# Optimization experiments

Measured on AMD Instinct MI355X. Metric: run time of the kernel, lower is better.

## Reference

```python
import jax, jax.numpy as jnp
import numpy as np

N = 50000; E = 800000; T = 800000; G = 64
H = 128; IEMB = 128; BAS = 8; NS = 4; NR = 6; OEH = 128; OUT = 1; NB = 4; CUT = 5.0


def envelope(x):
    # exponent=5 -> p=6: 1/x + a*x^5 + b*x^6 + c*x^7 with a=-28, b=48, c=-21
    return 1.0 / x - 28.0 * x**5 + 48.0 * x**6 - 21.0 * x**7


def setup_inputs() -> dict:
    key = jax.random.key(0)
    ks = iter(jax.random.split(key, 80))
    def w(shape, s=0.1):
        return jax.random.normal(next(ks), shape, dtype=jnp.float32) * s
    inp = {}
    inp['z'] = jax.random.randint(next(ks), (N,), 0, 100, dtype=jnp.int32)
    inp['dist'] = jax.random.uniform(next(ks), (E,), jnp.float32, 0.05, 1.0)
    inp['dist_trip'] = jax.random.uniform(next(ks), (T,), jnp.float32, 0.05, 1.0)
    inp['angle'] = jax.random.uniform(next(ks), (T,), jnp.float32, -1.0, 1.0)
    inp['edge_index'] = jax.random.randint(next(ks), (2, E), 0, N, dtype=jnp.int32)
    inp['triplets'] = jax.random.randint(next(ks), (T, 3), 0, N, dtype=jnp.int32)
    inp['batch'] = jnp.sort(jax.random.randint(next(ks), (N,), 0, G, dtype=jnp.int32))
    inp['atom_table'] = w((100, H), 1.0)
    inp['rbf_freq'] = jnp.arange(1, NR + 1, dtype=jnp.float32) * jnp.float32(np.pi)
    inp['sbf_freq'] = jnp.arange(1, NR + 1, dtype=jnp.float32) * jnp.float32(np.pi)
    inp['emb_w1'] = w((NR, IEMB)); inp['emb_b1'] = w((IEMB,), 0.01)
    inp['emb_w2'] = w((IEMB, H)); inp['emb_b2'] = w((H,), 0.01)
    inp['iw_rbf1'] = w((NB, NR, BAS)); inp['iw_rbf2'] = w((NB, BAS, H))
    inp['iw_sbf1'] = w((NB, NS * NR, BAS)); inp['iw_sbf2'] = w((NB, BAS, IEMB))
    inp['iw_t1'] = w((NB, H, IEMB)); inp['iw_t2'] = w((NB, IEMB, H)); inp['ib_t2'] = w((NB, H), 0.01)
    inp['iw_up'] = w((NB, H, H)); inp['ib_up'] = w((NB, H), 0.01)
    inp['iw_down'] = w((NB, H, H)); inp['ib_down'] = w((NB, H), 0.01)
    inp['ow_rbf'] = w((NB + 1, NR, H))
    inp['ow0'] = w((NB + 1, H, OEH)); inp['ob0'] = w((NB + 1, OEH), 0.01)
    inp['ow1'] = w((NB + 1, OEH, OEH)); inp['ob1'] = w((NB + 1, OEH), 0.01)
    inp['ow2'] = w((NB + 1, OEH, OUT)); inp['ob2'] = w((NB + 1, OUT), 0.01)
    return inp


def _forward(atom_table, rbf_freq, sbf_freq, emb_w1, emb_b1, emb_w2, emb_b2,
             iw_rbf1, iw_rbf2, iw_sbf1, iw_sbf2, iw_t1, iw_t2, ib_t2,
             iw_up, ib_up, iw_down, ib_down, ow_rbf, ow0, ob0, ow1, ob1, ow2, ob2,
             dist, dist_trip, angle, z, edge_index, triplets, batch):
    row, col = edge_index[0], edge_index[1]
    j_idx = triplets[:, 1]
    # radial basis for edges: [E, NR]
    d = dist[:, None] / CUT
    rbf_e = envelope(d) * jnp.sin(rbf_freq * d)
    # spherical basis for triplets: [T, NS*NR]
    dt = dist_trip[:, None] / CUT
    rbf_t = envelope(dt) * jnp.sin(sbf_freq * dt)
    a = angle[:, None]
    sph = jnp.concatenate([jnp.ones_like(a), a, 0.5 * (3 * a**2 - 1), 0.5 * (5 * a**3 - 3 * a)], axis=-1)
    sbf_t = (rbf_t[:, None, :] * sph[:, :, None]).reshape(a.shape[0], -1)

    x = atom_table[z]  # [N, H]
    # EmbeddingBlock: edge msg from rbf only, scattered to col
    e = jax.nn.silu(rbf_e @ emb_w1 + emb_b1) @ emb_w2 + emb_b2
    x = x + jax.ops.segment_sum(e, col, num_segments=N)

    def out_block(k, x):
        rbf_emb = rbf_e @ ow_rbf[k]            # [E, H]
        h = jax.ops.segment_sum(x[row] * rbf_emb, col, num_segments=N)
        h = jax.nn.silu(h @ ow0[k] + ob0[k])
        h = jax.nn.silu(h @ ow1[k] + ob1[k])
        return h @ ow2[k] + ob2[k]             # [N, OUT]

    P = out_block(0, x)
    for b in range(NB):
        x_up = x @ iw_up[b] + ib_up[b]
        x_down = x @ iw_down[b] + ib_down[b]
        rbf_emb = jax.nn.silu(rbf_e @ iw_rbf1[b]) @ iw_rbf2[b]      # [E, H]
        x_edge = x_up[row] * rbf_emb                                  # [E, H]
        sbf_emb = jax.nn.silu(sbf_t @ iw_sbf1[b]) @ iw_sbf2[b]      # [T, H]
        t = jax.nn.silu(x_down @ iw_t1[b]) @ iw_t2[b] + ib_t2[b]     # [N, H]
        # original: for each triplet i, x_edge += t[j]*sbf_emb[i] (broadcast over all edges)
        extra = jnp.sum(t[j_idx] * sbf_emb, axis=0)                   # [H]
        x_edge = x_edge + extra
        x = x + jax.ops.segment_sum(x_edge, col, num_segments=N)
        P = P + out_block(b + 1, x)

    counts = jax.ops.segment_sum(jnp.ones((x.shape[0],), jnp.float32), batch, num_segments=G)
    pooled = jax.ops.segment_sum(P, batch, num_segments=G) / jnp.maximum(counts, 1.0)[:, None]
    return pooled  # [G, OUT]


def reference(z, dist, dist_trip, angle, edge_index, triplets, batch, atom_table, rbf_freq, sbf_freq,
              emb_w1, emb_b1, emb_w2, emb_b2, iw_rbf1, iw_rbf2, iw_sbf1, iw_sbf2, iw_t1, iw_t2, ib_t2,
              iw_up, ib_up, iw_down, ib_down, ow_rbf, ow0, ob0, ow1, ob1, ow2, ob2):
    return _forward(atom_table, rbf_freq, sbf_freq, emb_w1, emb_b1, emb_w2, emb_b2,
                    iw_rbf1, iw_rbf2, iw_sbf1, iw_sbf2, iw_t1, iw_t2, ib_t2,
                    iw_up, ib_up, iw_down, ib_down, ow_rbf, ow0, ob0, ow1, ob1, ow2, ob2,
                    dist, dist_trip, angle, z, edge_index, triplets, batch)
```

## Files before the change

### kernel.cpp

```cpp
#include <hip/hip_runtime.h>
#include <hip/hip_fp16.h>

#define N_ 50000
#define E_ 800000
#define T_ 800000
#define G_ 64
#define H_ 128

#define NBK 782
#define NSB (NBK * 8)
#define CAPS 512
#define CHUNK 4096
#define EB ((E_ + CHUNK - 1) / CHUNK)
#define TB ((T_ + CHUNK - 1) / CHUNK)
#define XSLOT 16

#define GEMMG2 ((N_ + 31) / 32)
#define NG2 ((N_ + 1) / 2)
#define NIX ((N_ * 16 + 127) / 128)
#define SVG ((N_ + 3) / 4)
#define EG ((E_ + 255) / 256)
#define TG ((T_ + 255) / 256)

typedef __attribute__((ext_vector_type(8))) short bf16x8;
typedef __attribute__((ext_vector_type(4))) float f32x4;
typedef _Float16 f16x2 __attribute__((ext_vector_type(2)));

__device__ __forceinline__ float siluf(float v) {
    return __fdividef(v, 1.0f + __expf(-v));
}

__device__ __forceinline__ unsigned short f2bf(float f) {
    unsigned int u = __float_as_uint(f);
    u += 0x7fffu + ((u >> 16) & 1u);
    return (unsigned short)(u >> 16);
}
__device__ __forceinline__ unsigned int f2bf2(float a, float b) {
    return (unsigned int)f2bf(a) | ((unsigned int)f2bf(b) << 16);
}
__device__ __forceinline__ float bf2f(unsigned short h) {
    return __uint_as_float(((unsigned int)h) << 16);
}
__device__ __forceinline__ float2 bf2x2(unsigned int p) {
    return make_float2(__uint_as_float(p << 16), __uint_as_float(p & 0xffff0000u));
}
__device__ __forceinline__ float fdot2f(f16x2 a, f16x2 b, float c) {
    return __builtin_amdgcn_fdot2(a, b, c, false);
}

__global__ __launch_bounds__(256) void k_bucket(const int* __restrict__ ecol,
                                                const int* __restrict__ trip,
                                                int* bcntE, unsigned int* __restrict__ ebkt,
                                                int* bcntT, unsigned int* __restrict__ tbkt) {
    __shared__ int hist[NBK];
    __shared__ int bbase[NBK];
    int blk = blockIdx.x;
    bool isE = blk < EB;
    int ebase = (isE ? blk : blk - EB) * CHUNK;
    const int nElem = isE ? E_ : T_;
    int r = blk & 7;
    int* bcnt = isE ? bcntE : bcntT;
    unsigned int* bkt = isE ? ebkt : tbkt;
    int tid = threadIdx.x;

    for (int i = tid; i < NBK; i += 256) hist[i] = 0;
    __syncthreads();

    int cols[16];
    #pragma unroll
    for (int u = 0; u < 16; ++u) {
        int idx = ebase + u * 256 + tid;
        int c = -1;
        if (idx < nElem) c = isE ? ecol[idx] : trip[3 * idx + 1];
        cols[u] = c;
        if (c >= 0) atomicAdd(&hist[c >> 6], 1);
    }
    __syncthreads();

    for (int b = tid; b < NBK; b += 256) {
        int c = hist[b];
        bbase[b] = c ? atomicAdd(&bcnt[b * 8 + r], c) : 0;
        hist[b] = 0;
    }
    __syncthreads();

    #pragma unroll
    for (int u = 0; u < 16; ++u) {
        int c = cols[u];
        if (c >= 0) {
            int bk = c >> 6;
            int off = atomicAdd(&hist[bk], 1);
            int pos = bbase[bk] + off;
            if (pos < CAPS) {
                int idx = ebase + u * 256 + tid;
                bkt[(size_t)(bk * 8 + r) * CAPS + pos] =
                    ((unsigned int)idx << 6) | (unsigned int)(c & 63);
            }
        }
    }
}

// ... 143 lines not shown
        if (t >= T_) return;
        float2 da = tpay[t];
        float d = da.x * 0.2f;
        float a = da.y;
        float d2 = d * d, d4 = d2 * d2, d5 = d4 * d;
        float env = __fdividef(1.0f, d) - 28.0f * d5 + 48.0f * d5 * d - 21.0f * d5 * d2;
        float rb[6];
        #pragma unroll
        for (int r = 0; r < 6; ++r) rb[r] = env * __sinf(sfreq[r] * d);
        float sph[4];
        sph[0] = 1.0f; sph[1] = a; sph[2] = 1.5f * a * a - 0.5f; sph[3] = 2.5f * a * a * a - 1.5f * a;
        __half out[24];
        #pragma unroll
        for (int s = 0; s < 4; ++s)
            #pragma unroll
            for (int r = 0; r < 6; ++r) out[s * 6 + r] = __float2half(sph[s] * rb[r]);
        uint4* dst = (uint4*)(basis + (size_t)t * 24);
        dst[0] = ((uint4*)out)[0];
        dst[1] = ((uint4*)out)[1];
        dst[2] = ((uint4*)out)[2];
    }
}

__global__ __launch_bounds__(128) void k_embSix(const float* __restrict__ atab, const int* __restrict__ z,
                                                unsigned short* __restrict__ xh,
                                                const int* __restrict__ rowptr, const float* __restrict__ rbfS,
                                                const float* __restrict__ w1, const float* __restrict__ b1,
                                                unsigned short* __restrict__ SSh) {
    int tid = threadIdx.x;
    if (blockIdx.x < NIX) {
        int t = blockIdx.x * 128 + tid;
        if (t >= N_ * 16) return;
        int node = t >> 4, q = t & 15;
        const float4* a4 = (const float4*)atab;
        float4 v0 = a4[(size_t)z[node] * 32 + q * 2];
        float4 v1 = a4[(size_t)z[node] * 32 + q * 2 + 1];
        uint4 pk;
        pk.x = f2bf2(v0.x, v0.y);
        pk.y = f2bf2(v0.z, v0.w);
        pk.z = f2bf2(v1.x, v1.y);
        pk.w = f2bf2(v1.z, v1.w);
        ((uint4*)xh)[t] = pk;
    } else {
        int node = (blockIdx.x - NIX) * 2 + (tid >> 6);
        int lane = tid & 63;
        if (node >= N_) return;
        int c = lane * 2;
        float wc0[6], wc1[6];
        #pragma unroll
        for (int r = 0; r < 6; ++r) { wc0[r] = w1[r * 128 + c]; wc1[r] = w1[r * 128 + c + 1]; }
        float bb0 = b1[c], bb1 = b1[c + 1];
        float a0 = 0.f, a1 = 0.f;
        int p0 = rowptr[node], p1 = rowptr[node + 1];
        int p = p0;
        for (; p + 4 <= p1; p += 4) {
            float2 rb[4][3];
            #pragma unroll
            for (int u = 0; u < 4; ++u) {
                const float2* r2 = (const float2*)&rbfS[(size_t)(p + u) * 6];
                rb[u][0] = r2[0]; rb[u][1] = r2[1]; rb[u][2] = r2[2];
            }
            #pragma unroll
            for (int u = 0; u < 4; ++u) {
                float u0 = bb0 + rb[u][0].x * wc0[0] + rb[u][0].y * wc0[1] + rb[u][1].x * wc0[2] +
                           rb[u][1].y * wc0[3] + rb[u][2].x * wc0[4] + rb[u][2].y * wc0[5];
                float u1 = bb1 + rb[u][0].x * wc1[0] + rb[u][0].y * wc1[1] + rb[u][1].x * wc1[2] +
                           rb[u][1].y * wc1[3] + rb[u][2].x * wc1[4] + rb[u][2].y * wc1[5];
                a0 += siluf(u0);
                a1 += siluf(u1);
            }
        }
        for (; p < p1; ++p) {
            const float2* r2 = (const float2*)&rbfS[(size_t)p * 6];
            float2 ra = r2[0], rbx = r2[1], rc = r2[2];
            float u0 = bb0 + ra.x * wc0[0] + ra.y * wc0[1] + rbx.x * wc0[2] + rbx.y * wc0[3] + rc.x * wc0[4] + rc.y * wc0[5];
            float u1 = bb1 + ra.x * wc1[0] + ra.y * wc1[1] + rbx.x * wc1[2] + rbx.y * wc1[3] + rc.x * wc1[4] + rc.y * wc1[5];
            a0 += siluf(u0);
            a1 += siluf(u1);
        }
        *(unsigned int*)&SSh[(size_t)node * 128 + c] = f2bf2(a0, a1);
    }
}


__device__ __forceinline__ void body_gemm(int bid, const unsigned short* Ap, const unsigned short* Wt,
                                          const float* bias, const int* rp, unsigned short* Ch, int M) {
    int tid = threadIdx.x;
    int wave = tid >> 6, lane = tid & 63;
    int m15 = lane & 15, quad = lane >> 4;
    int row0 = bid * 32 + wave * 16;
    int arow = row0 + m15;
    if (arow > M - 1) arow = M - 1;

    f32x4 acc[8];
    #pragma unroll
    for (int nt = 0; nt < 8; ++nt) acc[nt] = (f32x4){0.f, 0.f, 0.f, 0.f};
    #pragma unroll
    for (int kt = 0; kt < 4; ++kt) {
        int ks = kt * 32 + quad * 8;
        bf16x8 av = *(const bf16x8*)(Ap + (size_t)arow * 128 + ks);
        #pragma unroll
        for (int nt = 0; nt < 8; ++nt) {
            bf16x8 bf = *(const bf16x8*)(Wt + (size_t)(nt * 16 + m15) * 128 + ks);
            acc[nt] = __builtin_amdgcn_mfma_f32_16x16x32_bf16(av, bf, acc[nt], 0, 0, 0);
        }
    }
    #pragma unroll
    for (int nt = 0; nt < 8; ++nt) {
        int col = nt * 16 + m15;
        float bc = bias[col];
        #pragma unroll
        for (int reg = 0; reg < 4; ++reg) {
            int row = row0 + quad * 4 + reg;
            if (row < M) {
                float v = acc[nt][reg] + bc * (float)(rp[row + 1] - rp[row]);
                v += bf2f(Ch[(size_t)row * 128 + col]);
                Ch[(size_t)row * 128 + col] = f2bf(v);
            }
        }
    }
}

__device__ __forceinline__ void body_sv4(int bid, const int* rowptrT, const __half* basis,
                                         const float* iw_sbf1, float* SV4, int n) {
    int tid = threadIdx.x;
    int wave = tid >> 6, lane = tid & 63;
    int node = bid * 4 + wave * 2 + (lane >> 5);
    int sub = lane & 31;
    int blk = sub >> 3, k = sub & 7;
    if (node >= n) return;
    const float* W1 = iw_sbf1 + blk * 192;
    f16x2 w[12];
    #pragma unroll
    for (int j = 0; j < 12; ++j) {
        f16x2 t;
        t.x = (_Float16)W1[(2 * j) * 8 + k];
        t.y = (_Float16)W1[(2 * j + 1) * 8 + k];
        w[j] = t;
    }
    float acc = 0.f;
    int p0 = rowptrT[node], p1 = rowptrT[node + 1];
    for (int p = p0; p < p1; ++p) {
        union { uint4 q[3]; f16x2 h[12]; } bs;
        const uint4* bp = (const uint4*)(basis + (size_t)p * 24);
        bs.q[0] = bp[0]; bs.q[1] = bp[1]; bs.q[2] = bp[2];
        float u = 0.f;
        #pragma unroll
        for (int j = 0; j < 12; ++j) u = fdot2f(bs.h[j], w[j], u);
        acc += siluf(u);
    }
    SV4[((size_t)blk * n + node) * 8 + k] = acc;
}

__device__ __forceinline__ void body_gather(int node0, const int* rowptr, const int* slist,
                                            const float* rbfS, const unsigned short* xh,
                                            const float* wrbf, unsigned short* hB, int n) {
    int tid = threadIdx.x;
    int node = node0 + (tid >> 6);
    int lane = tid & 63;
    if (node >= n) return;
    int c = lane * 2;
    float wc0[6], wc1[6];
    #pragma unroll
    for (int r = 0; r < 6; ++r) { wc0[r] = wrbf[r * 128 + c]; wc1[r] = wrbf[r * 128 + c + 1]; }
    float a0 = 0.f, a1 = 0.f;
    int p0 = rowptr[node], p1 = rowptr[node + 1];
    int p = p0;
    for (; p + 4 <= p1; p += 4) {
        int s0 = slist[p], s1 = slist[p + 1], s2 = slist[p + 2], s3 = slist[p + 3];
        float2 rb[4][3];
        #pragma unroll
        for (int u = 0; u < 4; ++u) {
            const float2* r2 = (const float2*)&rbfS[(size_t)(p + u) * 6];
            rb[u][0] = r2[0]; rb[u][1] = r2[1]; rb[u][2] = r2[2];
        }
        unsigned int xv0 = *(const unsigned int*)&xh[(size_t)s0 * 128 + c];
        unsigned int xv1 = *(const unsigned int*)&xh[(size_t)s1 * 128 + c];
        unsigned int xv2 = *(const unsigned int*)&xh[(size_t)s2 * 128 + c];
        unsigned int xv3 = *(const unsigned int*)&xh[(size_t)s3 * 128 + c];
        #pragma unroll
        for (int u = 0; u < 4; ++u) {
            float e0 = rb[u][0].x * wc0[0] + rb[u][0].y * wc0[1] + rb[u][1].x * wc0[2] +
                       rb[u][1].y * wc0[3] + rb[u][2].x * wc0[4] + rb[u][2].y * wc0[5];
            float e1 = rb[u][0].x * wc1[0] + rb[u][0].y * wc1[1] + rb[u][1].x * wc1[2] +
                       rb[u][1].y * wc1[3] + rb[u][2].x * wc1[4] + rb[u][2].y * wc1[5];
            float2 xf = bf2x2((u == 0) ? xv0 : (u == 1) ? xv1 : (u == 2) ? xv2 : xv3);
            a0 += xf.x * e0;
            a1 += xf.y * e1;
        }
    }
    for (; p < p1; ++p) {
        int src = slist[p];
        const float2* r2 = (const float2*)&rbfS[(size_t)p * 6];
        float2 ra = r2[0], rbx = r2[1], rc = r2[2];
        float e0 = ra.x * wc0[0] + ra.y * wc0[1] + rbx.x * wc0[2] + rbx.y * wc0[3] + rc.x * wc0[4] + rc.y * wc0[5];
        float e1 = ra.x * wc1[0] + ra.y * wc1[1] + rbx.x * wc1[2] + rbx.y * wc1[3] + rc.x * wc1[4] + rc.y * wc1[5];
        float2 xf = bf2x2(*(const unsigned int*)&xh[(size_t)src * 128 + c]);
        a0 += xf.x * e0;
        a1 += xf.y * e1;
    }
    *(unsigned int*)&hB[(size_t)node * 128 + c] = f2bf2(a0, a1);
}

__device__ __forceinline__ void body_block_mlp(int bid, unsigned short* smh,
                                               const unsigned short* xh,
                                               const unsigned short* Wd, const float* bd,
                                               const unsigned short* Wt1,
                                               const unsigned short* Wt2, const float* bt2,
                                               const unsigned short* Wup, const float* bup,
                                               const float* SV, const float* W2,
                                               float* extraP, unsigned short* xuph, int M) {
    int tid = threadIdx.x;
    int wave = tid >> 6, lane = tid & 63;
    int m15 = lane & 15, quad = lane >> 4;
    int row0 = bid * 32 + wave * 16;
    int arow = row0 + m15;
    if (arow > M - 1) arow = M - 1;
    unsigned short* L = smh + wave * (16 * 136);

    f32x4 accD[8], accU[8];
    #pragma unroll
    for (int nt = 0; nt < 8; ++nt) { accD[nt] = (f32x4){0.f, 0.f, 0.f, 0.f}; accU[nt] = (f32x4){0.f, 0.f, 0.f, 0.f}; }
    #pragma unroll
    for (int kt = 0; kt < 4; ++kt) {
        int ks = kt * 32 + quad * 8;
        bf16x8 av = *(const bf16x8*)(xh + (size_t)arow * 128 + ks);
        #pragma unroll
        for (int nt = 0; nt < 8; ++nt) {
            bf16x8 bd_ = *(const bf16x8*)(Wd + (size_t)(nt * 16 + m15) * 128 + ks);
            accD[nt] = __builtin_amdgcn_mfma_f32_16x16x32_bf16(av, bd_, accD[nt], 0, 0, 0);
            bf16x8 bu_ = *(const bf16x8*)(Wup + (size_t)(nt * 16 + m15) * 128 + ks);
            accU[nt] = __builtin_amdgcn_mfma_f32_16x16x32_bf16(av, bu_, accU[nt], 0, 0, 0);
        }
    }
    #pragma unroll
    for (int nt = 0; nt < 8; ++nt) {
        int col = nt * 16 + m15;
        float bcu = bup[col], bcd = bd[col];
        #pragma unroll
        for (int reg = 0; reg < 4; ++reg) {
            int row = row0 + quad * 4 + reg;
            if (row < M) xuph[(size_t)row * 128 + col] = f2bf(accU[nt][reg] + bcu);
            L[(quad * 4 + reg) * 136 + col] = f2bf(accD[nt][reg] + bcd);
        }
    }
    __syncthreads();

    #pragma unroll
    for (int nt = 0; nt < 8; ++nt) accD[nt] = (f32x4){0.f, 0.f, 0.f, 0.f};
    #pragma unroll
    for (int kt = 0; kt < 4; ++kt) {
        int ks = kt * 32 + quad * 8;
        bf16x8 av = *(const bf16x8*)(L + m15 * 136 + ks);
        #pragma unroll
        for (int nt = 0; nt < 8; ++nt) {
            bf16x8 bf = *(const bf16x8*)(Wt1 + (size_t)(nt * 16 + m15) * 128 + ks);
            accD[nt] = __builtin_amdgcn_mfma_f32_16x16x32_bf16(av, bf, accD[nt], 0, 0, 0);
        }
    }
    __syncthreads();
    #pragma unroll
    for (int nt = 0; nt < 8; ++nt) {
        int col = nt * 16 + m15;
        #pragma unroll
        for (int reg = 0; reg < 4; ++reg)
            L[(quad * 4 + reg) * 136 + col] = f2bf(siluf(accD[nt][reg]));
    }
    __syncthreads();

    #pragma unroll
    for (int nt = 0; nt < 8; ++nt) accD[nt] = (f32x4){0.f, 0.f, 0.f, 0.f};
    #pragma unroll
    for (int kt = 0; kt < 4; ++kt) {
        int ks = kt * 32 + quad * 8;
        bf16x8 av = *(const bf16x8*)(L + m15 * 136 + ks);
        #pragma unroll
        for (int nt = 0; nt < 8; ++nt) {
            bf16x8 bf = *(const bf16x8*)(Wt2 + (size_t)(nt * 16 + m15) * 128 + ks);
            accD[nt] = __builtin_amdgcn_mfma_f32_16x16x32_bf16(av, bf, accD[nt], 0, 0, 0);
        }
    }
    __syncthreads();
    #pragma unroll
    for (int nt = 0; nt < 8; ++nt) {
        int col = nt * 16 + m15;
        float bc = bt2[col];
        #pragma unroll
        for (int reg = 0; reg < 4; ++reg)
            smh[(wave * 16 + quad * 4 + reg) * 136 + col] = f2bf(accD[nt][reg] + bc);
    }
    __syncthreads();

    int col = tid;
    float acc8[8];
    #pragma unroll
    for (int k = 0; k < 8; ++k) acc8[k] = 0.f;
    int rmax = M - bid * 32;
    if (rmax > 32) rmax = 32;
    for (int rr = 0; rr < rmax; ++rr) {
        float t = bf2f(smh[rr * 136 + col]);
        const float4* sv4 = (const float4*)&SV[(size_t)(bid * 32 + rr) * 8];
        float4 s0 = sv4[0], s1 = sv4[1];
        acc8[0] += t * s0.x; acc8[1] += t * s0.y; acc8[2] += t * s0.z; acc8[3] += t * s0.w;
        acc8[4] += t * s1.x; acc8[5] += t * s1.y; acc8[6] += t * s1.z; acc8[7] += t * s1.w;
    }
    float e = 0.f;
    #pragma unroll
    for (int k = 0; k < 8; ++k) e += acc8[k] * W2[k * 128 + col];
    atomicAdd(&extraP[(bid & (XSLOT - 1)) * 128 + col], e);
}

template <int PACC>
__device__ __forceinline__ void body_out_mlp(int bid, unsigned short* smh,
                                             const unsigned short* hB,
                                             const unsigned short* W0t, const float* b0,
                                             const unsigned short* W1t, const float* b1,
                                             const float* w2col, const float* ob2p,
                                             float* Pout, int M) {
    int tid = threadIdx.x;
    int wave = tid >> 6, lane = tid & 63;
    int m15 = lane & 15, quad = lane >> 4;
    int row0 = bid * 32 + wave * 16;
    int arow = row0 + m15;
    if (arow > M - 1) arow = M - 1;
    unsigned short* L = smh + wave * (16 * 136);

    f32x4 acc[8];
    #pragma unroll
    for (int nt = 0; nt < 8; ++nt) acc[nt] = (f32x4){0.f, 0.f, 0.f, 0.f};
    #pragma unroll
    for (int kt = 0; kt < 4; ++kt) {
        int ks = kt * 32 + quad * 8;
        bf16x8 av = *(const bf16x8*)(hB + (size_t)arow * 128 + ks);
        #pragma unroll
        for (int nt = 0; nt < 8; ++nt) {
            bf16x8 bf = *(const bf16x8*)(W0t + (size_t)(nt * 16 + m15) * 128 + ks);
            acc[nt] = __builtin_amdgcn_mfma_f32_16x16x32_bf16(av, bf, acc[nt], 0, 0, 0);
        }
    }
    #pragma unroll
    for (int nt = 0; nt < 8; ++nt) {
        int col = nt * 16 + m15;
        float bc = b0[col];
        #pragma unroll
        for (int reg = 0; reg < 4; ++reg)
            L[(quad * 4 + reg) * 136 + col] = f2bf(siluf(acc[nt][reg] + bc));
    }
    __syncthreads();

    #pragma unroll
    for (int nt = 0; nt < 8; ++nt) acc[nt] = (f32x4){0.f, 0.f, 0.f, 0.f};
    #pragma unroll
    for (int kt = 0; kt < 4; ++kt) {
        int ks = kt * 32 + quad * 8;
        bf16x8 av = *(const bf16x8*)(L + m15 * 136 + ks);
        #pragma unroll
        for (int nt = 0; nt < 8; ++nt) {
            bf16x8 bf = *(const bf16x8*)(W1t + (size_t)(nt * 16 + m15) * 128 + ks);
            acc[nt] = __builtin_amdgcn_mfma_f32_16x16x32_bf16(av, bf, acc[nt], 0, 0, 0);
        }
    }
    float w2c[8], pp[4];
    #pragma unroll
    for (int nt = 0; nt < 8; ++nt) w2c[nt] = w2col[nt * 16 + m15];
    #pragma unroll
    for (int reg = 0; reg < 4; ++reg) pp[reg] = 0.f;
    #pragma unroll
    for (int nt = 0; nt < 8; ++nt) {
        float bc = b1[nt * 16 + m15];
        #pragma unroll
        for (int reg = 0; reg < 4; ++reg)
            pp[reg] += siluf(acc[nt][reg] + bc) * w2c[nt];
    }
    #pragma unroll
    for (int reg = 0; reg < 4; ++reg) {
        float s = pp[reg];
        s += __shfl_xor(s, 1, 64);
        s += __shfl_xor(s, 2, 64);
        s += __shfl_xor(s, 4, 64);
        s += __shfl_xor(s, 8, 64);
        if (m15 == 0) {
            int row = row0 + quad * 4 + reg;
            if (row < M) {
                float r = s + ob2p[0];
                if (PACC == 2) r += Pout[row];
                Pout[row] = r;
            }
        }
    }
}

__device__ __forceinline__ void body_interact(int node0, float* exs,
                                              const int* rowptr, const int* slist,
                                              const __half* s8, const float* W2,
                                              const float* extraP,
                                              const unsigned short* xuph,
                                              unsigned short* xh, int n) {
    int tid = threadIdx.x;
    {
        float s = 0.f;
        #pragma unroll
        for (int q = 0; q < XSLOT; ++q) s += extraP[q * 128 + tid];
        exs[tid] = s;
    }
    __syncthreads();
    int node = node0 + (tid >> 6);
    int lane = tid & 63;
    if (node >= n) return;
    int c = lane * 2;
    f16x2 w2a[4], w2b[4];
    #pragma unroll
    for (int j = 0; j < 4; ++j) {
        f16x2 wa, wb;
        wa.x = (_Float16)W2[(2 * j) * 128 + c];
        wa.y = (_Float16)W2[(2 * j + 1) * 128 + c];
        wb.x = (_Float16)W2[(2 * j) * 128 + c + 1];
        wb.y = (_Float16)W2[(2 * j + 1) * 128 + c + 1];
        w2a[j] = wa;
        w2b[j] = wb;
    }
    int p0 = rowptr[node], p1 = rowptr[node + 1];
    float cntf = (float)(p1 - p0);
    float a0 = cntf * exs[c], a1 = cntf * exs[c + 1];
    int p = p0;
    for (; p + 4 <= p1; p += 4) {
        int s0 = slist[p], s1 = slist[p + 1], s2 = slist[p + 2], s3 = slist[p + 3];
        uint4 sv[4];
        #pragma unroll
        for (int u = 0; u < 4; ++u) sv[u] = *(const uint4*)(s8 + (size_t)(p + u) * 8);
        unsigned int xv0 = *(const unsigned int*)&xuph[(size_t)s0 * 128 + c];
        unsigned int xv1 = *(const unsigned int*)&xuph[(size_t)s1 * 128 + c];
        unsigned int xv2 = *(const unsigned int*)&xuph[(size_t)s2 * 128 + c];
        unsigned int xv3 = *(const unsigned int*)&xuph[(size_t)s3 * 128 + c];
        #pragma unroll
        for (int u = 0; u < 4; ++u) {
            union { uint4 q; f16x2 h[4]; } s;
            s.q = sv[u];
            float e0 = fdot2f(s.h[0], w2a[0], 0.f);
            e0 = fdot2f(s.h[1], w2a[1], e0);
            e0 = fdot2f(s.h[2], w2a[2], e0);
            e0 = fdot2f(s.h[3], w2a[3], e0);
            float e1 = fdot2f(s.h[0], w2b[0], 0.f);
            e1 = fdot2f(s.h[1], w2b[1], e1);
            e1 = fdot2f(s.h[2], w2b[2], e1);
            e1 = fdot2f(s.h[3], w2b[3], e1);
            float2 xf = bf2x2((u == 0) ? xv0 : (u == 1) ? xv1 : (u == 2) ? xv2 : xv3);
            a0 += xf.x * e0;
            a1 += xf.y * e1;
        }
    }
    for (; p < p1; ++p) {
        int src = slist[p];
        float2 xf = bf2x2(*(const unsigned int*)&xuph[(size_t)src * 128 + c]);
        union { uint4 q; f16x2 h[4]; } s;
        s.q = *(const uint4*)(s8 + (size_t)p * 8);
        float e0 = fdot2f(s.h[0], w2a[0], 0.f);
        e0 = fdot2f(s.h[1], w2a[1], e0);
        e0 = fdot2f(s.h[2], w2a[2], e0);
        e0 = fdot2f(s.h[3], w2a[3], e0);
        float e1 = fdot2f(s.h[0], w2b[0], 0.f);
        e1 = fdot2f(s.h[1], w2b[1], e1);
        e1 = fdot2f(s.h[2], w2b[2], e1);
        e1 = fdot2f(s.h[3], w2b[3], e1);
        a0 += xf.x * e0;
        a1 += xf.y * e1;
    }
    unsigned int cur = *(unsigned int*)&xh[(size_t)node * 128 + c];
    float2 xc = bf2x2(cur);
    *(unsigned int*)&xh[(size_t)node * 128 + c] = f2bf2(xc.x + a0, xc.y + a1);
}


__global__ __launch_bounds__(128) void k_gemmsv(const unsigned short* __restrict__ Ap,
                                                const unsigned short* __restrict__ Wt,
                                                const float* __restrict__ bias, const int* __restrict__ rp,
                                                unsigned short* __restrict__ Ch,
                                                const int* __restrict__ rowptrT, const __half* __restrict__ basis,
                                                const float* __restrict__ iw_sbf1, float* __restrict__ SV4) {
    if (blockIdx.x < GEMMG2)
        body_gemm(blockIdx.x, Ap, Wt, bias, rp, Ch, N_);
    else
        body_sv4(blockIdx.x - GEMMG2, rowptrT, basis, iw_sbf1, SV4, N_);
}

__global__ __launch_bounds__(128) void k_fuse_gb(const unsigned short* __restrict__ xh,
                                                 const unsigned short* __restrict__ Wd, const float* __restrict__ bd,
                                                 const unsigned short* __restrict__ Wt1,
                                                 const unsigned short* __restrict__ Wt2, const float* __restrict__ bt2,
                                                 const unsigned short* __restrict__ Wup, const float* __restrict__ bup,
                                                 const float* __restrict__ SV, const float* __restrict__ W2,
                                                 float* __restrict__ extraP, unsigned short* __restrict__ xuph,
                                                 const int* __restrict__ rowptr, const int* __restrict__ slist,
                                                 const float* __restrict__ rbfS, const float* __restrict__ wrbf,
                                                 unsigned short* __restrict__ hB) {
    __shared__ unsigned short smh[2 * 16 * 136];
    if (blockIdx.x < GEMMG2)
        body_block_mlp(blockIdx.x, smh, xh, Wd, bd, Wt1, Wt2, bt2, Wup, bup, SV, W2, extraP, xuph, N_);
    else
        body_gather((blockIdx.x - GEMMG2) * 2, rowptr, slist, rbfS, xh, wrbf, hB, N_);
}

template <int PACC>
__global__ __launch_bounds__(128) void k_fuse_mi(const unsigned short* __restrict__ hB,
                                                 const unsigned short* __restrict__ W0t, const float* __restrict__ b0,
                                                 const unsigned short* __restrict__ W1t, const float* __restrict__ b1,
                                                 const float* __restrict__ w2col, const float* __restrict__ ob2p,
                                                 float* __restrict__ Pout,
                                                 const int* __restrict__ rowptr, const int* __restrict__ slist,
                                                 const __half* __restrict__ s8, const float* __restrict__ W2,
                                                 const float* __restrict__ extraP,
                                                 const unsigned short* __restrict__ xuph,
                                                 unsigned short* __restrict__ xh) {
    __shared__ unsigned short smh[2 * 16 * 136];
    if (blockIdx.x < GEMMG2)
        body_out_mlp<PACC>(blockIdx.x, smh, hB, W0t, b0, W1t, b1, w2col, ob2p, Pout, N_);
    else
        body_interact((blockIdx.x - GEMMG2) * 2, (float*)smh, rowptr, slist, s8, W2, extraP, xuph, xh, N_);
}

__global__ __launch_bounds__(128) void k_gather1(const int* __restrict__ rowptr, const int* __restrict__ slist,
                                                 const float* __restrict__ rbfS, const unsigned short* __restrict__ xh,
                                                 const float* __restrict__ wrbf, unsigned short* __restrict__ hB) {
    body_gather(blockIdx.x * 2, rowptr, slist, rbfS, xh, wrbf, hB, N_);
}
__global__ __launch_bounds__(128) void k_mlp1(const unsigned short* __restrict__ hB,
                                              const unsigned short* __restrict__ W0t, const float* __restrict__ b0,
                                              const unsigned short* __restrict__ W1t, const float* __restrict__ b1,
                                              const float* __restrict__ w2col, const float* __restrict__ ob2p,
                                              float* __restrict__ Pout) {
    __shared__ unsigned short smh[2 * 16 * 136];
    body_out_mlp<2>(blockIdx.x, smh, hB, W0t, b0, W1t, b1, w2col, ob2p, Pout, N_);
}

__global__ __launch_bounds__(256) void k_pool(const float* __restrict__ P, const int* __restrict__ batch,
                                              float* __restrict__ pool, float* __restrict__ cnt, int n) {
    int i = blockIdx.x * 256 + threadIdx.x;
    int lane = threadIdx.x & 63;
    int b = (i < n) ? batch[i] : -1;
    float p = (i < n) ? P[i] : 0.f;
    int b0 = __shfl(b, 0, 64);
    int b63 = __shfl(b, 63, 64);
    if (b0 == b63 && b0 >= 0) {
        float s = p;
        #pragma unroll
        for (int off = 32; off > 0; off >>= 1) s += __shfl_xor(s, off, 64);
        if (lane == 0) {
            atomicAdd(&pool[b0], s);
            atomicAdd(&cnt[b0], 64.0f);
        }
    } else {
        if (i < n) {
            atomicAdd(&pool[b], p);
            atomicAdd(&cnt[b], 1.0f);
        }
    }
}

__global__ __launch_bounds__(64) void k_final(const float* __restrict__ pool, const float* __restrict__ cnt,
                                              float* __restrict__ out) {
    int g = threadIdx.x;
    if (g < G_) out[g] = __fdividef(pool[g], fmaxf(cnt[g], 1.0f));
}

extern "C" void kernel_launch(void* const* d_in, const int* in_sizes, int n_in,
                              void* d_out, int out_size, void* d_ws, size_t ws_size,
                              hipStream_t stream) {
    (void)in_sizes; (void)n_in; (void)out_size; (void)ws_size;
    const int* z = (const int*)d_in[0];
    const float* dist = (const float*)d_in[1];
    const float* dist_trip = (const float*)d_in[2];
    const float* angle = (const float*)d_in[3];
    const int* edge_index = (const int*)d_in[4];
    const int* triplets = (const int*)d_in[5];
    const int* batch = (const int*)d_in[6];
    const float* atom_table = (const float*)d_in[7];
    const float* rbf_freq = (const float*)d_in[8];
    const float* sbf_freq = (const float*)d_in[9];
    const float* emb_w1 = (const float*)d_in[10];
    const float* emb_b1 = (const float*)d_in[11];
    const float* emb_w2 = (const float*)d_in[12];
    const float* emb_b2 = (const float*)d_in[13];
    const float* iw_rbf1 = (const float*)d_in[14];
    const float* iw_rbf2 = (const float*)d_in[15];
    const float* iw_sbf1 = (const float*)d_in[16];
    const float* iw_sbf2 = (const float*)d_in[17];
    const float* iw_t1 = (const float*)d_in[18];
    const float* iw_t2 = (const float*)d_in[19];
    const float* ib_t2 = (const float*)d_in[20];
    const float* iw_up = (const float*)d_in[21];
    const float* ib_up = (const float*)d_in[22];
    const float* iw_down = (const float*)d_in[23];
    const float* ib_down = (const float*)d_in[24];
    const float* ow_rbf = (const float*)d_in[25];
    const float* ow0 = (const float*)d_in[26];
    const float* ob0 = (const float*)d_in[27];
    const float* ow1 = (const float*)d_in[28];
    const float* ob1 = (const float*)d_in[29];
    const float* ow2 = (const float*)d_in[30];
    const float* ob2 = (const float*)d_in[31];

    const int* erow = edge_index;
    const int* ecol = edge_index + E_;

    float* ws = (float*)d_ws;
    float* bufA = ws;
    float* bufB = bufA + (size_t)N_ * H_;
    float* P = bufB + (size_t)N_ * H_;
    float* rbfS = P + N_;
    float* SV4 = rbfS + (size_t)E_ * 6;
    float* extra4 = SV4 + (size_t)4 * N_ * 8;
    float* pool = extra4 + 4 * XSLOT * 128;
    float* cnt = pool + G_;
    int* bcntE = (int*)(cnt + G_);
    int* bcntT = bcntE + NSB;
    int* bktbaseE = bcntT + NSB;
    int* bktbaseT = bktbaseE + NBK;
    int* rowptr = bktbaseT + NBK;
    int* rowptrT = rowptr + N_ + 1;
    int* slist = rowptrT + N_ + 1;
    float* distS = (float*)(slist + E_);
    uintptr_t tp = (uintptr_t)(distS + E_);
    tp = (tp + 7) & ~(uintptr_t)7;
    float2* tpay = (float2*)tp;
    __half* s8all = (__half*)(tpay + T_);
    __half* basis = s8all + (size_t)4 * E_ * 8;
    unsigned short* xh = (unsigned short*)(basis + (size_t)T_ * 24);
    unsigned short* xuph = xh + (size_t)N_ * H_;
    unsigned short* Wt = xuph + (size_t)N_ * H_;
    unsigned short* hB = (unsigned short*)bufB;

    unsigned int* ebkt = (unsigned int*)s8all;
    unsigned int* tbkt = ebkt + (size_t)NSB * CAPS;

    hipMemsetAsync(extra4, 0, (4 * XSLOT * 128 + 2 * G_ + 2 * NSB) * sizeof(float), stream);
    k_wprep<<<27 * 8, 256, 0, stream>>>(emb_w2, iw_down, iw_t1, iw_t2, iw_up, ow0, ow1, Wt);
    k_bucket<<<EB + TB, 256, 0, stream>>>(ecol, triplets, bcntE, ebkt, bcntT, tbkt);
    k_scanB<<<2, 1024, 0, stream>>>(bcntE, bktbaseE, bcntT, bktbaseT);
    k_place<<<2 * NBK, 256, 0, stream>>>(bcntE, ebkt, erow, dist, bktbaseE, rowptr, slist, distS,
                                         bcntT, tbkt, dist_trip, angle, bktbaseT, rowptrT, tpay);

    k_geomb<<<EG + TG, 256, 0, stream>>>(distS, rbf_freq, iw_rbf1, rbfS, s8all,
                                         tpay, sbf_freq, basis);
    k_embSix<<<NIX + NG2, 128, 0, stream>>>(atom_table, z, xh, rowptr, rbfS, emb_w1, emb_b1,
                                            (unsigned short*)bufA);
    k_gemmsv<<<GEMMG2 + SVG, 128, 0, stream>>>((unsigned short*)bufA, Wt, emb_b2, rowptr, xh,
                                               rowptrT, basis, iw_sbf1, SV4);

    for (int b = 0; b < 4; ++b) {
        k_fuse_gb<<<GEMMG2 + NG2, 128, 0, stream>>>(xh,
                                                    Wt + (size_t)(1 + b) * 16384, ib_down + b * 128,
                                                    Wt + (size_t)(5 + b) * 16384,
                                                    Wt + (size_t)(9 + b) * 16384, ib_t2 + b * 128,
                                                    Wt + (size_t)(13 + b) * 16384, ib_up + b * 128,
                                                    SV4 + (size_t)b * N_ * 8,
                                                    iw_sbf2 + (size_t)b * 1024,
                                                    extra4 + (size_t)b * XSLOT * 128,
                                                    xuph,
                                                    rowptr, slist, rbfS,
                                                    ow_rbf + (size_t)b * 6 * 128, hB);
        if (b == 0)
            k_fuse_mi<1><<<GEMMG2 + NG2, 128, 0, stream>>>(hB,
                                                           Wt + (size_t)(17 + b) * 16384, ob0 + b * 128,
                                                           Wt + (size_t)(22 + b) * 16384, ob1 + b * 128,
                                                           ow2 + b * 128, ob2 + b, P,
                                                           rowptr, slist, s8all + (size_t)b * E_ * 8,
                                                           iw_rbf2 + (size_t)b * 1024,
                                                           extra4 + (size_t)b * XSLOT * 128,
                                                           xuph, xh);
        else
            k_fuse_mi<2><<<GEMMG2 + NG2, 128, 0, stream>>>(hB,
                                                           Wt + (size_t)(17 + b) * 16384, ob0 + b * 128,
                                                           Wt + (size_t)(22 + b) * 16384, ob1 + b * 128,
                                                           ow2 + b * 128, ob2 + b, P,
                                                           rowptr, slist, s8all + (size_t)b * E_ * 8,
                                                           iw_rbf2 + (size_t)b * 1024,
                                                           extra4 + (size_t)b * XSLOT * 128,
                                                           xuph, xh);
    }

    k_gather1<<<NG2, 128, 0, stream>>>(rowptr, slist, rbfS, xh, ow_rbf + (size_t)4 * 6 * 128, hB);
    k_mlp1<<<GEMMG2, 128, 0, stream>>>(hB, Wt + (size_t)21 * 16384, ob0 + 4 * 128,
                                       Wt + (size_t)26 * 16384, ob1 + 4 * 128,
                                       ow2 + 4 * 128, ob2 + 4, P);

    k_pool<<<(N_ + 255) / 256, 256, 0, stream>>>(P, batch, pool, cnt, N_);
    k_final<<<1, 64, 0, stream>>>(pool, cnt, (float*)d_out);
}
```

Measured before the change: 1.533 ms.

## Unfuse block kernels into separate gather, MLP and interact launches with deeper unroll

Splits the horizontally fused kernels (block MLP plus output gather, output MLP plus interaction) into standalone kernels and reorders the schedule so each output block runs right after its interaction. The gather and interact kernels move to 256-thread blocks covering 4 nodes and add an 8-way unrolled edge loop so more independent loads are in flight. The aim is to avoid the mismatched-work blocks in the fused launches hurting occupancy and register allocation. In exchange it adds kernel launches per block and gives up the concurrency the fused launches provided.

```diff
diff --git a/kernel.cpp b/kernel.cpp
--- a/kernel.cpp
+++ b/kernel.cpp
@@ -17,6 +17,7 @@
 
 #define GEMMG2 ((N_ + 31) / 32)
 #define NG2 ((N_ + 1) / 2)
+#define NG4 ((N_ + 3) / 4)
 #define NIX ((N_ * 16 + 127) / 128)
 #define SVG ((N_ + 3) / 4)
 #define EG ((E_ + 255) / 256)
@@ -326,7 +327,6 @@
     }
 }
 
-
 __device__ __forceinline__ void body_gemm(int bid, const unsigned short* Ap, const unsigned short* Wt,
                                           const float* bias, const int* rp, unsigned short* Ch, int M) {
     int tid = threadIdx.x;
@@ -396,64 +396,28 @@
     SV4[((size_t)blk * n + node) * 8 + k] = acc;
 }
 
-__device__ __forceinline__ void body_gather(int node0, const int* rowptr, const int* slist,
-                                            const float* rbfS, const unsigned short* xh,
-                                            const float* wrbf, unsigned short* hB, int n) {
-    int tid = threadIdx.x;
-    int node = node0 + (tid >> 6);
-    int lane = tid & 63;
-    if (node >= n) return;
-    int c = lane * 2;
-    float wc0[6], wc1[6];
-    #pragma unroll
-    for (int r = 0; r < 6; ++r) { wc0[r] = wrbf[r * 128 + c]; wc1[r] = wrbf[r * 128 + c + 1]; }
-    float a0 = 0.f, a1 = 0.f;
-    int p0 = rowptr[node], p1 = rowptr[node + 1];
-    int p = p0;
-    for (; p + 4 <= p1; p += 4) {
-        int s0 = slist[p], s1 = slist[p + 1], s2 = slist[p + 2], s3 = slist[p + 3];
-        float2 rb[4][3];
-        #pragma unroll
-        for (int u = 0; u < 4; ++u) {
-            const float2* r2 = (const float2*)&rbfS[(size_t)(p + u) * 6];
-            rb[u][0] = r2[0]; rb[u][1] = r2[1]; rb[u][2] = r2[2];
-        }
-        unsigned int xv0 = *(const unsigned int*)&xh[(size_t)s0 * 128 + c];
-        unsigned int xv1 = *(const unsigned int*)&xh[(size_t)s1 * 128 + c];
-        unsigned int xv2 = *(const unsigned int*)&xh[(size_t)s2 * 128 + c];
-        unsigned int xv3 = *(const unsigned int*)&xh[(size_t)s3 * 128 + c];
-        #pragma unroll
-        for (int u = 0; u < 4; ++u) {
-            float e0 = rb[u][0].x * wc0[0] + rb[u][0].y * wc0[1] + rb[u][1].x * wc0[2] +
-                       rb[u][1].y * wc0[3] + rb[u][2].x * wc0[4] + rb[u][2].y * wc0[5];
-            float e1 = rb[u][0].x * wc1[0] + rb[u][0].y * wc1[1] + rb[u][1].x * wc1[2] +
-                       rb[u][1].y * wc1[3] + rb[u][2].x * wc1[4] + rb[u][2].y * wc1[5];
-            float2 xf = bf2x2((u == 0) ? xv0 : (u == 1) ? xv1 : (u == 2) ? xv2 : xv3);
-            a0 += xf.x * e0;
-            a1 += xf.y * e1;
-        }
-    }
-    for (; p < p1; ++p) {
-        int src = slist[p];
-        const float2* r2 = (const float2*)&rbfS[(size_t)p * 6];
-        float2 ra = r2[0], rbx = r2[1], rc = r2[2];
-        float e0 = ra.x * wc0[0] + ra.y * wc0[1] + rbx.x * wc0[2] + rbx.y * wc0[3] + rc.x * wc0[4] + rc.y * wc0[5];
-        float e1 = ra.x * wc1[0] + ra.y * wc1[1] + rbx.x * wc1[2] + rbx.y * wc1[3] + rc.x * wc1[4] + rc.y * wc1[5];
-        float2 xf = bf2x2(*(const unsigned int*)&xh[(size_t)src * 128 + c]);
-        a0 += xf.x * e0;
-        a1 += xf.y * e1;
-    }
-    *(unsigned int*)&hB[(size_t)node * 128 + c] = f2bf2(a0, a1);
-}
-
-__device__ __forceinline__ void body_block_mlp(int bid, unsigned short* smh,
-                                               const unsigned short* xh,
-                                               const unsigned short* Wd, const float* bd,
-                                               const unsigned short* Wt1,
-                                               const unsigned short* Wt2, const float* bt2,
-                                               const unsigned short* Wup, const float* bup,
-                                               const float* SV, const float* W2,
-                                               float* extraP, unsigned short* xuph, int M) {
+__global__ __launch_bounds__(128) void k_gemmsv(const unsigned short* __restrict__ Ap,
+                                                const unsigned short* __restrict__ Wt,
+                                                const float* __restrict__ bias, const int* __restrict__ rp,
+                                                unsigned short* __restrict__ Ch,
+                                                const int* __restrict__ rowptrT, const __half* __restrict__ basis,
+                                                const float* __restrict__ iw_sbf1, float* __restrict__ SV4) {
+    if (blockIdx.x < GEMMG2)
+        body_gemm(blockIdx.x, Ap, Wt, bias, rp, Ch, N_);
+    else
+        body_sv4(blockIdx.x - GEMMG2, rowptrT, basis, iw_sbf1, SV4, N_);
+}
+
+__global__ __launch_bounds__(128) void k_block_mlp(const unsigned short* __restrict__ xh,
+                                                   const unsigned short* __restrict__ Wd, const float* __restrict__ bd,
+                                                   const unsigned short* __restrict__ Wt1,
+                                                   const unsigned short* __restrict__ Wt2, const float* __restrict__ bt2,
+                                                   const unsigned short* __restrict__ Wup, const float* __restrict__ bup,
+                                                   const float* __restrict__ SV, const float* __restrict__ W2,
+                                                   float* __restrict__ extraP,
+                                                   unsigned short* __restrict__ xuph, int M) {
+    __shared__ unsigned short smh[2 * 16 * 136];
+    int bid = blockIdx.x;
     int tid = threadIdx.x;
     int wave = tid >> 6, lane = tid & 63;
     int m15 = lane & 15, quad = lane >> 4;
@@ -555,19 +519,19 @@
 }
 
 template <int PACC>
-__device__ __forceinline__ void body_out_mlp(int bid, unsigned short* smh,
-                                             const unsigned short* hB,
-                                             const unsigned short* W0t, const float* b0,
-                                             const unsigned short* W1t, const float* b1,
-                                             const float* w2col, const float* ob2p,
-                                             float* Pout, int M) {
+__global__ __launch_bounds__(128) void k_out_mlp(const unsigned short* __restrict__ hB,
+                                                 const unsigned short* __restrict__ W0t, const float* __restrict__ b0,
+                                                 const unsigned short* __restrict__ W1t, const float* __restrict__ b1,
+                                                 const float* __restrict__ w2col, const float* __restrict__ ob2p,
+                                                 float* __restrict__ Pout, int M) {
+    __shared__ unsigned short lds[2][16 * 136];
     int tid = threadIdx.x;
     int wave = tid >> 6, lane = tid & 63;
     int m15 = lane & 15, quad = lane >> 4;
-    int row0 = bid * 32 + wave * 16;
+    int row0 = blockIdx.x * 32 + wave * 16;
     int arow = row0 + m15;
     if (arow > M - 1) arow = M - 1;
-    unsigned short* L = smh + wave * (16 * 136);
+    unsigned short* L = lds[wave];
 
     f32x4 acc[8];
     #pragma unroll
@@ -627,28 +591,104 @@
             int row = row0 + quad * 4 + reg;
             if (row < M) {
                 float r = s + ob2p[0];
-                if (PACC == 2) r += Pout[row];
+                if constexpr (PACC == 2) r += Pout[row];
                 Pout[row] = r;
             }
         }
     }
 }
 
-__device__ __forceinline__ void body_interact(int node0, float* exs,
-                                              const int* rowptr, const int* slist,
-                                              const __half* s8, const float* W2,
-                                              const float* extraP,
-                                              const unsigned short* xuph,
-                                              unsigned short* xh, int n) {
+__global__ __launch_bounds__(256) void k_out_gather(const int* __restrict__ rowptr, const int* __restrict__ slist,
+                                                    const float* __restrict__ rbfS,
+                                                    const unsigned short* __restrict__ xh,
+                                                    const float* __restrict__ wrbf,
+                                                    unsigned short* __restrict__ hB, int n) {
+    int node = blockIdx.x * 4 + (threadIdx.x >> 6);
+    int lane = threadIdx.x & 63;
+    if (node >= n) return;
+    int c = lane * 2;
+    float wc0[6], wc1[6];
+    #pragma unroll
+    for (int r = 0; r < 6; ++r) { wc0[r] = wrbf[r * 128 + c]; wc1[r] = wrbf[r * 128 + c + 1]; }
+    float a0 = 0.f, a1 = 0.f;
+    int p0 = rowptr[node], p1 = rowptr[node + 1];
+    int p = p0;
+    for (; p + 8 <= p1; p += 8) {
+        int ss[8];
+        #pragma unroll
+        for (int u = 0; u < 8; ++u) ss[u] = slist[p + u];
+        unsigned int xv[8];
+        #pragma unroll
+        for (int u = 0; u < 8; ++u) xv[u] = *(const unsigned int*)&xh[(size_t)ss[u] * 128 + c];
+        float2 rb[8][3];
+        #pragma unroll
+        for (int u = 0; u < 8; ++u) {
+            const float2* r2 = (const float2*)&rbfS[(size_t)(p + u) * 6];
+            rb[u][0] = r2[0]; rb[u][1] = r2[1]; rb[u][2] = r2[2];
+        }
+        #pragma unroll
+        for (int u = 0; u < 8; ++u) {
+            float e0 = rb[u][0].x * wc0[0] + rb[u][0].y * wc0[1] + rb[u][1].x * wc0[2] +
+                       rb[u][1].y * wc0[3] + rb[u][2].x * wc0[4] + rb[u][2].y * wc0[5];
+            float e1 = rb[u][0].x * wc1[0] + rb[u][0].y * wc1[1] + rb[u][1].x * wc1[2] +
+                       rb[u][1].y * wc1[3] + rb[u][2].x * wc1[4] + rb[u][2].y * wc1[5];
+            float2 xf = bf2x2(xv[u]);
+            a0 += xf.x * e0;
+            a1 += xf.y * e1;
+        }
+    }
+    for (; p + 4 <= p1; p += 4) {
+        int ss[4];
+        #pragma unroll
+        for (int u = 0; u < 4; ++u) ss[u] = slist[p + u];
+        unsigned int xv[4];
+        #pragma unroll
+        for (int u = 0; u < 4; ++u) xv[u] = *(const unsigned int*)&xh[(size_t)ss[u] * 128 + c];
+        float2 rb[4][3];
+        #pragma unroll
+        for (int u = 0; u < 4; ++u) {
+            const float2* r2 = (const float2*)&rbfS[(size_t)(p + u) * 6];
+            rb[u][0] = r2[0]; rb[u][1] = r2[1]; rb[u][2] = r2[2];
+        }
+        #pragma unroll
+        for (int u = 0; u < 4; ++u) {
+            float e0 = rb[u][0].x * wc0[0] + rb[u][0].y * wc0[1] + rb[u][1].x * wc0[2] +
+                       rb[u][1].y * wc0[3] + rb[u][2].x * wc0[4] + rb[u][2].y * wc0[5];
+            float e1 = rb[u][0].x * wc1[0] + rb[u][0].y * wc1[1] + rb[u][1].x * wc1[2] +
+                       rb[u][1].y * wc1[3] + rb[u][2].x * wc1[4] + rb[u][2].y * wc1[5];
+            float2 xf = bf2x2(xv[u]);
+            a0 += xf.x * e0;
+            a1 += xf.y * e1;
+        }
+    }
+    for (; p < p1; ++p) {
+        int src = slist[p];
+        const float2* r2 = (const float2*)&rbfS[(size_t)p * 6];
+        float2 ra = r2[0], rbx = r2[1], rc = r2[2];
+        float e0 = ra.x * wc0[0] + ra.y * wc0[1] + rbx.x * wc0[2] + rbx.y * wc0[3] + rc.x * wc0[4] + rc.y * wc0[5];
+        float e1 = ra.x * wc1[0] + ra.y * wc1[1] + rbx.x * wc1[2] + rbx.y * wc1[3] + rc.x * wc1[4] + rc.y * wc1[5];
+        float2 xf = bf2x2(*(const unsigned int*)&xh[(size_t)src * 128 + c]);
+        a0 += xf.x * e0;
+        a1 += xf.y * e1;
+    }
+    *(unsigned int*)&hB[(size_t)node * 128 + c] = f2bf2(a0, a1);
+}
+
+__global__ __launch_bounds__(256) void k_interact(const int* __restrict__ rowptr, const int* __restrict__ slist,
+                                                  const __half* __restrict__ s8, const float* __restrict__ W2,
+                                                  const float* __restrict__ extraP,
+                                                  const unsigned short* __restrict__ xuph,
+                                                  unsigned short* __restrict__ xh, int n) {
+    __shared__ float exs[128];
     int tid = threadIdx.x;
-    {
+    if (tid < 128) {
         float s = 0.f;
         #pragma unroll
         for (int q = 0; q < XSLOT; ++q) s += extraP[q * 128 + tid];
         exs[tid] = s;
     }
     __syncthreads();
-    int node = node0 + (tid >> 6);
+    int node = blockIdx.x * 4 + (tid >> 6);
     int lane = tid & 63;
     if (node >= n) return;
     int c = lane * 2;
@@ -667,15 +707,43 @@
     float cntf = (float)(p1 - p0);
     float a0 = cntf * exs[c], a1 = cntf * exs[c + 1];
     int p = p0;
+    for (; p + 8 <= p1; p += 8) {
+        int ss[8];
+        #pragma unroll
+        for (int u = 0; u < 8; ++u) ss[u] = slist[p + u];
+        unsigned int xv[8];
+        #pragma unroll
+        for (int u = 0; u < 8; ++u) xv[u] = *(const unsigned int*)&xuph[(size_t)ss[u] * 128 + c];
+        uint4 sv[8];
+        #pragma unroll
+        for (int u = 0; u < 8; ++u) sv[u] = *(const uint4*)(s8 + (size_t)(p + u) * 8);
+        #pragma unroll
+        for (int u = 0; u < 8; ++u) {
+            union { uint4 q; f16x2 h[4]; } s;
+            s.q = sv[u];
+            float e0 = fdot2f(s.h[0], w2a[0], 0.f);
+            e0 = fdot2f(s.h[1], w2a[1], e0);
+            e0 = fdot2f(s.h[2], w2a[2], e0);
+            e0 = fdot2f(s.h[3], w2a[3], e0);
+            float e1 = fdot2f(s.h[0], w2b[0], 0.f);
+            e1 = fdot2f(s.h[1], w2b[1], e1);
+            e1 = fdot2f(s.h[2], w2b[2], e1);
+            e1 = fdot2f(s.h[3], w2b[3], e1);
+            float2 xf = bf2x2(xv[u]);
+            a0 += xf.x * e0;
+            a1 += xf.y * e1;
+        }
+    }
     for (; p + 4 <= p1; p += 4) {
-        int s0 = slist[p], s1 = slist[p + 1], s2 = slist[p + 2], s3 = slist[p + 3];
+        int ss[4];
+        #pragma unroll
+        for (int u = 0; u < 4; ++u) ss[u] = slist[p + u];
+        unsigned int xv[4];
+        #pragma unroll
+        for (int u = 0; u < 4; ++u) xv[u] = *(const unsigned int*)&xuph[(size_t)ss[u] * 128 + c];
         uint4 sv[4];
         #pragma unroll
         for (int u = 0; u < 4; ++u) sv[u] = *(const uint4*)(s8 + (size_t)(p + u) * 8);
-        unsigned int xv0 = *(const unsigned int*)&xuph[(size_t)s0 * 128 + c];
-        unsigned int xv1 = *(const unsigned int*)&xuph[(size_t)s1 * 128 + c];
-        unsigned int xv2 = *(const unsigned int*)&xuph[(size_t)s2 * 128 + c];
-        unsigned int xv3 = *(const unsigned int*)&xuph[(size_t)s3 * 128 + c];
         #pragma unroll
         for (int u = 0; u < 4; ++u) {
             union { uint4 q; f16x2 h[4]; } s;
@@ -688,7 +756,7 @@
             e1 = fdot2f(s.h[1], w2b[1], e1);
             e1 = fdot2f(s.h[2], w2b[2], e1);
             e1 = fdot2f(s.h[3], w2b[3], e1);
-            float2 xf = bf2x2((u == 0) ? xv0 : (u == 1) ? xv1 : (u == 2) ? xv2 : xv3);
+            float2 xf = bf2x2(xv[u]);
             a0 += xf.x * e0;
             a1 += xf.y * e1;
         }
@@ -712,68 +780,6 @@
     unsigned int cur = *(unsigned int*)&xh[(size_t)node * 128 + c];
     float2 xc = bf2x2(cur);
     *(unsigned int*)&xh[(size_t)node * 128 + c] = f2bf2(xc.x + a0, xc.y + a1);
-}
-
-
-__global__ __launch_bounds__(128) void k_gemmsv(const unsigned short* __restrict__ Ap,
-                                                const unsigned short* __restrict__ Wt,
-                                                const float* __restrict__ bias, const int* __restrict__ rp,
-                                                unsigned short* __restrict__ Ch,
-                                                const int* __restrict__ rowptrT, const __half* __restrict__ basis,
-                                                const float* __restrict__ iw_sbf1, float* __restrict__ SV4) {
-    if (blockIdx.x < GEMMG2)
-        body_gemm(blockIdx.x, Ap, Wt, bias, rp, Ch, N_);
-    else
-        body_sv4(blockIdx.x - GEMMG2, rowptrT, basis, iw_sbf1, SV4, N_);
-}
-
-__global__ __launch_bounds__(128) void k_fuse_gb(const unsigned short* __restrict__ xh,
-                                                 const unsigned short* __restrict__ Wd, const float* __restrict__ bd,
-                                                 const unsigned short* __restrict__ Wt1,
-                                                 const unsigned short* __restrict__ Wt2, const float* __restrict__ bt2,
-                                                 const unsigned short* __restrict__ Wup, const float* __restrict__ bup,
-                                                 const float* __restrict__ SV, const float* __restrict__ W2,
-                                                 float* __restrict__ extraP, unsigned short* __restrict__ xuph,
-                                                 const int* __restrict__ rowptr, const int* __restrict__ slist,
-                                                 const float* __restrict__ rbfS, const float* __restrict__ wrbf,
-                                                 unsigned short* __restrict__ hB) {
-    __shared__ unsigned short smh[2 * 16 * 136];
-    if (blockIdx.x < GEMMG2)
-        body_block_mlp(blockIdx.x, smh, xh, Wd, bd, Wt1, Wt2, bt2, Wup, bup, SV, W2, extraP, xuph, N_);
-    else
-        body_gather((blockIdx.x - GEMMG2) * 2, rowptr, slist, rbfS, xh, wrbf, hB, N_);
-}
-
-template <int PACC>
-__global__ __launch_bounds__(128) void k_fuse_mi(const unsigned short* __restrict__ hB,
-                                                 const unsigned short* __restrict__ W0t, const float* __restrict__ b0,
-                                                 const unsigned short* __restrict__ W1t, const float* __restrict__ b1,
-                                                 const float* __restrict__ w2col, const float* __restrict__ ob2p,
-                                                 float* __restrict__ Pout,
-                                                 const int* __restrict__ rowptr, const int* __restrict__ slist,
-                                                 const __half* __restrict__ s8, const float* __restrict__ W2,
-                                                 const float* __restrict__ extraP,
-                                                 const unsigned short* __restrict__ xuph,
-                                                 unsigned short* __restrict__ xh) {
-    __shared__ unsigned short smh[2 * 16 * 136];
-    if (blockIdx.x < GEMMG2)
-        body_out_mlp<PACC>(blockIdx.x, smh, hB, W0t, b0, W1t, b1, w2col, ob2p, Pout, N_);
-    else
-        body_interact((blockIdx.x - GEMMG2) * 2, (float*)smh, rowptr, slist, s8, W2, extraP, xuph, xh, N_);
-}
-
-__global__ __launch_bounds__(128) void k_gather1(const int* __restrict__ rowptr, const int* __restrict__ slist,
-                                                 const float* __restrict__ rbfS, const unsigned short* __restrict__ xh,
-                                                 const float* __restrict__ wrbf, unsigned short* __restrict__ hB) {
-    body_gather(blockIdx.x * 2, rowptr, slist, rbfS, xh, wrbf, hB, N_);
-}
-__global__ __launch_bounds__(128) void k_mlp1(const unsigned short* __restrict__ hB,
-                                              const unsigned short* __restrict__ W0t, const float* __restrict__ b0,
-                                              const unsigned short* __restrict__ W1t, const float* __restrict__ b1,
-                                              const float* __restrict__ w2col, const float* __restrict__ ob2p,
-                                              float* __restrict__ Pout) {
-    __shared__ unsigned short smh[2 * 16 * 136];
-    body_out_mlp<2>(blockIdx.x, smh, hB, W0t, b0, W1t, b1, w2col, ob2p, Pout, N_);
 }
 
 __global__ __launch_bounds__(256) void k_pool(const float* __restrict__ P, const int* __restrict__ batch,
@@ -890,42 +896,36 @@
     k_gemmsv<<<GEMMG2 + SVG, 128, 0, stream>>>((unsigned short*)bufA, Wt, emb_b2, rowptr, xh,
                                                rowptrT, basis, iw_sbf1, SV4);
 
+    auto out_block = [&](int k, bool first) {
+        k_out_gather<<<NG4, 256, 0, stream>>>(rowptr, slist, rbfS, xh,
+                                              ow_rbf + (size_t)k * 6 * 128, hB, N_);
+        if (first)
+            k_out_mlp<1><<<GEMMG2, 128, 0, stream>>>(hB, Wt + (size_t)(17 + k) * 16384, ob0 + k * 128,
+                                                     Wt + (size_t)(22 + k) * 16384, ob1 + k * 128,
+                                                     ow2 + k * 128, ob2 + k, P, N_);
+        else
+            k_out_mlp<2><<<GEMMG2, 128, 0, stream>>>(hB, Wt + (size_t)(17 + k) * 16384, ob0 + k * 128,
+                                                     Wt + (size_t)(22 + k) * 16384, ob1 + k * 128,
+                                                     ow2 + k * 128, ob2 + k, P, N_);
+    };
+
+    out_block(0, true);
+
     for (int b = 0; b < 4; ++b) {
-        k_fuse_gb<<<GEMMG2 + NG2, 128, 0, stream>>>(xh,
-                                                    Wt + (size_t)(1 + b) * 16384, ib_down + b * 128,
-                                                    Wt + (size_t)(5 + b) * 16384,
-                                                    Wt + (size_t)(9 + b) * 16384, ib_t2 + b * 128,
-                                                    Wt + (size_t)(13 + b) * 16384, ib_up + b * 128,
-                                                    SV4 + (size_t)b * N_ * 8,
-                                                    iw_sbf2 + (size_t)b * 1024,
-                                                    extra4 + (size_t)b * XSLOT * 128,
-                                                    xuph,
-                                                    rowptr, slist, rbfS,
-                                                    ow_rbf + (size_t)b * 6 * 128, hB);
-        if (b == 0)
-            k_fuse_mi<1><<<GEMMG2 + NG2, 128, 0, stream>>>(hB,
-                                                           Wt + (size_t)(17 + b) * 16384, ob0 + b * 128,
-                                                           Wt + (size_t)(22 + b) * 16384, ob1 + b * 128,
-                                                           ow2 + b * 128, ob2 + b, P,
-                                                           rowptr, slist, s8all + (size_t)b * E_ * 8,
-                                                           iw_rbf2 + (size_t)b * 1024,
-                                                           extra4 + (size_t)b * XSLOT * 128,
-                                                           xuph, xh);
-        else
-            k_fuse_mi<2><<<GEMMG2 + NG2, 128, 0, stream>>>(hB,
-                                                           Wt + (size_t)(17 + b) * 16384, ob0 + b * 128,
-                                                           Wt + (size_t)(22 + b) * 16384, ob1 + b * 128,
-                                                           ow2 + b * 128, ob2 + b, P,
-                                                           rowptr, slist, s8all + (size_t)b * E_ * 8,
-                                                           iw_rbf2 + (size_t)b * 1024,
-                                                           extra4 + (size_t)b * XSLOT * 128,
-                                                           xuph, xh);
-    }
-
-    k_gather1<<<NG2, 128, 0, stream>>>(rowptr, slist, rbfS, xh, ow_rbf + (size_t)4 * 6 * 128, hB);
-    k_mlp1<<<GEMMG2, 128, 0, stream>>>(hB, Wt + (size_t)21 * 16384, ob0 + 4 * 128,
-                                       Wt + (size_t)26 * 16384, ob1 + 4 * 128,
-                                       ow2 + 4 * 128, ob2 + 4, P);
+        k_block_mlp<<<GEMMG2, 128, 0, stream>>>(xh,
+                                                Wt + (size_t)(1 + b) * 16384, ib_down + b * 128,
+                                                Wt + (size_t)(5 + b) * 16384,
+                                                Wt + (size_t)(9 + b) * 16384, ib_t2 + b * 128,
+                                                Wt + (size_t)(13 + b) * 16384, ib_up + b * 128,
+                                                SV4 + (size_t)b * N_ * 8,
+                                                iw_sbf2 + (size_t)b * 1024,
+                                                extra4 + (size_t)b * XSLOT * 128,
+                                                xuph, N_);
+        k_interact<<<NG4, 256, 0, stream>>>(rowptr, slist, s8all + (size_t)b * E_ * 8,
+                                            iw_rbf2 + (size_t)b * 1024, extra4 + (size_t)b * XSLOT * 128,
+                                            xuph, xh, N_);
+        out_block(b + 1, false);
+    }
 
     k_pool<<<(N_ + 255) / 256, 256, 0, stream>>>(P, batch, pool, cnt, N_);
     k_final<<<1, 64, 0, stream>>>(pool, cnt, (float*)d_out);
```

New measurement: 1.468 ms. 4.2% less time.
